# Optimization experiments

Hardware: AMD Instinct MI355X
Metric: run time of the kernel (lower is better)

## Reference

```python
import jax, jax.numpy as jnp
import numpy as np
from jax import lax

B = 16
A = 3
LEVEL_HW = [(200, 200), (100, 100), (50, 50), (25, 25)]
STRIDES = [4, 8, 16, 32]
SIZES = [32.0, 64.0, 128.0, 256.0]
RATIOS = np.array([0.5, 1.0, 2.0])
IMG_H = IMG_W = 800.0
PRE_NMS = 1000          # pre_nms_top_n (testing), applied per level
POST_NMS = 1000         # post_nms_top_n (testing)
NMS_THRESH = 0.7
SCORE_THRESH = 0.0
MIN_SIZE = 1.0
BBOX_XFORM_CLIP = float(np.log(1000.0 / 16.0))  # torchvision BoxCoder clamp
N_PER_LEVEL = [h * w * A for h, w in LEVEL_HW]


def _make_anchors():
    # torchvision-style grid anchors, per-location order matches (H, W, A) flatten
    out = []
    for (h, w), stride, size in zip(LEVEL_HW, STRIDES, SIZES):
        hr = np.sqrt(RATIOS)
        wr = 1.0 / hr
        ws = size * wr
        hs = size * hr
        base = np.stack([-ws / 2, -hs / 2, ws / 2, hs / 2], axis=1)  # [A,4]
        sx = np.arange(w) * stride
        sy = np.arange(h) * stride
        yy, xx = np.meshgrid(sy, sx, indexing="ij")
        shifts = np.stack([xx, yy, xx, yy], axis=-1).reshape(-1, 1, 4)
        out.append((shifts + base[None]).reshape(-1, 4))
    return np.concatenate(out, 0).astype(np.float32)


def setup_inputs():
    key = jax.random.key(0)
    ks = jax.random.split(key, 8)
    inp = {}
    for i, (h, w) in enumerate(LEVEL_HW):
        inp[f"cls{i}"] = jax.random.normal(ks[i], (B, A, h, w), jnp.float32)
        inp[f"reg{i}"] = jax.random.normal(ks[4 + i], (B, A * 4, h, w), jnp.float32)
    inp["anchors"] = jnp.asarray(_make_anchors())
    return inp


def _flat(layer, C):
    # permute_and_flatten: [N, A*C, H, W] -> [N, H*W*A, C]
    n, ac, h, w = layer.shape
    a = ac // C
    return layer.reshape(n, a, C, h, w).transpose(0, 3, 4, 1, 2).reshape(n, h * w * a, C)


def _forward(cls_list, reg_list, anchors):
    obj = jnp.concatenate([_flat(c, 1)[..., 0] for c in cls_list], axis=1)   # [B, K]
    deltas = jnp.concatenate([_flat(r, 4) for r in reg_list], axis=1)        # [B, K, 4]

    # --- BoxCoder.decode, weights (1,1,1,1) ---
    wa = anchors[:, 2] - anchors[:, 0]
    ha = anchors[:, 3] - anchors[:, 1]
    cxa = anchors[:, 0] + 0.5 * wa
    cya = anchors[:, 1] + 0.5 * ha
    dx, dy = deltas[..., 0], deltas[..., 1]
    dw = jnp.minimum(deltas[..., 2], BBOX_XFORM_CLIP)
    dh = jnp.minimum(deltas[..., 3], BBOX_XFORM_CLIP)
    pcx = dx * wa + cxa
    pcy = dy * ha + cya
    pw = jnp.exp(dw) * wa
    ph = jnp.exp(dh) * ha
    props = jnp.stack([pcx - 0.5 * pw, pcy - 0.5 * ph,
                       pcx + 0.5 * pw, pcy + 0.5 * ph], -1)  # [B, K, 4]

    # --- per-level top-k (pre_nms_top_n) ---
    idxs = []
    off = 0
    for n in N_PER_LEVEL:
        k = min(PRE_NMS, n)
        _, ti = lax.top_k(obj[:, off:off + n], k)
        idxs.append(ti + off)
        off += n
    top_idx = jnp.concatenate(idxs, axis=1)  # [B, Nc]
    lvl_full = jnp.concatenate([jnp.full((n,), i, jnp.int32)
                                for i, n in enumerate(N_PER_LEVEL)])
    scores = jax.nn.sigmoid(jnp.take_along_axis(obj, top_idx, axis=1))
    boxes = jnp.take_along_axis(props, top_idx[..., None], axis=1)
    lvl = lvl_full[top_idx]

    # --- clip to image, remove small boxes / score threshold (as validity mask) ---
    x1 = jnp.clip(boxes[..., 0], 0.0, IMG_W)
    y1 = jnp.clip(boxes[..., 1], 0.0, IMG_H)
    x2 = jnp.clip(boxes[..., 2], 0.0, IMG_W)
    y2 = jnp.clip(boxes[..., 3], 0.0, IMG_H)
    boxes = jnp.stack([x1, y1, x2, y2], -1)
    valid = (x2 - x1 >= MIN_SIZE) & (y2 - y1 >= MIN_SIZE) & (scores >= SCORE_THRESH)

    # --- sort by score desc (invalid ranked last) ---
    key = jnp.where(valid, scores, -1.0)
    order = jnp.argsort(-key, axis=1)
    boxes = jnp.take_along_axis(boxes, order[..., None], axis=1)
    scores = jnp.take_along_axis(scores, order, axis=1)
    lvl = jnp.take_along_axis(lvl, order, axis=1)
    valid = jnp.take_along_axis(valid, order, axis=1)

    # --- batched_nms: offset boxes by level so cross-level IoU = 0 ---
    off_mult = max(IMG_H, IMG_W) + 1.0
    boff = boxes + lvl[..., None].astype(boxes.dtype) * off_mult
    areas = (boff[..., 2] - boff[..., 0]) * (boff[..., 3] - boff[..., 1])  # [B, Nc]
    Nc = boff.shape[1]
    pos = jnp.arange(Nc)

    def step(supp, i):
        bi = boff[:, i]                                   # [B, 4]
        keep_i = valid[:, i] & (~supp[:, i])              # [B]
        ix1 = jnp.maximum(boff[..., 0], bi[:, None, 0])
        iy1 = jnp.maximum(boff[..., 1], bi[:, None, 1])
        ix2 = jnp.minimum(boff[..., 2], bi[:, None, 2])
        iy2 = jnp.minimum(boff[..., 3], bi[:, None, 3])
        inter = jnp.maximum(ix2 - ix1, 0.0) * jnp.maximum(iy2 - iy1, 0.0)
        union = areas + areas[:, i][:, None] - inter
        iou = inter / jnp.where(union > 0, union, 1.0)
        sup = keep_i[:, None] & (iou > NMS_THRESH) & (pos > i)[None, :]
        return supp | sup, keep_i

    _, keeps = lax.scan(step, jnp.zeros((boxes.shape[0], Nc), bool), pos)
    keep = keeps.T  # [B, Nc]

    # --- compact kept boxes (already score-sorted) into fixed [B, POST_NMS, ...] ---
    def sel(b, s, k):
        rank = jnp.cumsum(k) - 1
        idx = jnp.where(k & (rank < POST_NMS), rank, POST_NMS)  # overflow -> slot POST
        ob = jnp.zeros((POST_NMS + 1, 4), b.dtype).at[idx].set(b)[:POST_NMS]
        osc = jnp.zeros((POST_NMS + 1,), s.dtype).at[idx].set(s)[:POST_NMS]
        return ob, osc

    return jax.vmap(sel)(boxes, scores, keep)


def reference(cls0, cls1, cls2, cls3, reg0, reg1, reg2, reg3, anchors):
    return _forward([cls0, cls1, cls2, cls3], [reg0, reg1, reg2, reg3], anchors)
```

## Files before the change

### kernel.cpp

```cpp
#include <hip/hip_runtime.h>
#include <cstdint>
#include <cstddef>

typedef uint32_t u32;
typedef uint64_t u64;

#define NB 16
#define POSTN 1000
#define PREN 1000
#define LSEG 1024
#define LCH 16
#define SIDECAP 4096
#define BSIDE 2048
#define TRIPCAP (LSEG * LCH)
#define NPAIR 160
#define NBUCK 8192
#define BSHIFT 19

__constant__ int c_N[4]    = {120000, 30000, 7500, 1875};
__constant__ int c_OFF[4]  = {0, 120000, 150000, 157500};
__constant__ int c_HW[4]   = {40000, 10000, 2500, 625};
__constant__ int c_W[4]    = {200, 100, 50, 25};
__constant__ int c_BASE[4] = {0, 1024, 2048, 3072};

__device__ __forceinline__ u32 ord_bits(float f) {
  u32 u = __float_as_uint(f);
  return (u & 0x80000000u) ? ~u : (u | 0x80000000u);
}
__device__ __forceinline__ float inv_ord(u32 o) {
  u32 bits = (o & 0x80000000u) ? (o ^ 0x80000000u) : ~o;
  return __uint_as_float(bits);
}
__device__ __forceinline__ u64 readlane_u64(u64 v, int l) {
  u32 lo = (u32)__builtin_amdgcn_readlane((int)(u32)v, l);
  u32 hi = (u32)__builtin_amdgcn_readlane((int)(u32)(v >> 32), l);
  return (((u64)hi) << 32) | (u64)lo;
}

__device__ __forceinline__ void slice_map(int bid, int& lvl, int& b, int& e0,
                                          int& nsl) {
  if (bid < 128)      { lvl = 0; b = bid >> 3; e0 = (bid & 7) * 15000; nsl = 15000; }
  else if (bid < 160) { lvl = 1; int t = bid - 128; b = t >> 1; e0 = (t & 1) * 15000; nsl = 15000; }
  else if (bid < 176) { lvl = 2; b = bid - 160; e0 = 0; nsl = 7500; }
  else                { lvl = 3; b = bid - 176; e0 = 0; nsl = 1875; }
}

struct DecBox { float x1, y1, x2, y2; int lvl; bool valid; };

__device__ DecBox decode_box(u32 gid, int b,
    const float* __restrict__ reg0, const float* __restrict__ reg1,
    const float* __restrict__ reg2, const float* __restrict__ reg3,
    const float* __restrict__ anchors) {
  int lvl = (gid < 120000u) ? 0 : (gid < 150000u) ? 1 : (gid < 157500u) ? 2 : 3;
  int local = (int)gid - c_OFF[lvl];
  int a = local % 3;
  int cell = local / 3;
  int w = c_W[lvl];
  int hw = c_HW[lvl];
  int y = cell / w;
  int x = cell - y * w;
  const float* reg = (lvl == 0) ? reg0 : (lvl == 1) ? reg1 : (lvl == 2) ? reg2 : reg3;
  size_t base = ((size_t)(b * 12 + a * 4) * (size_t)w + (size_t)y) * (size_t)w + (size_t)x;
  const float CLIPV = 4.135166556742356f;
  float dx = reg[base];
  float dy = reg[base + (size_t)hw];
  float dwv = fminf(reg[base + 2 * (size_t)hw], CLIPV);
  float dhv = fminf(reg[base + 3 * (size_t)hw], CLIPV);
  float a0 = anchors[(size_t)gid * 4 + 0];
  float a1 = anchors[(size_t)gid * 4 + 1];
  float a2 = anchors[(size_t)gid * 4 + 2];
  float a3 = anchors[(size_t)gid * 4 + 3];
  float wa = __fsub_rn(a2, a0);
  float ha = __fsub_rn(a3, a1);
  float cxa = __fadd_rn(a0, __fmul_rn(0.5f, wa));
  float cya = __fadd_rn(a1, __fmul_rn(0.5f, ha));
  float pcx = __fadd_rn(__fmul_rn(dx, wa), cxa);
  float pcy = __fadd_rn(__fmul_rn(dy, ha), cya);
  float pw = __fmul_rn(expf(dwv), wa);
  float ph = __fmul_rn(expf(dhv), ha);
  float x1 = __fsub_rn(pcx, __fmul_rn(0.5f, pw));
  float y1 = __fsub_rn(pcy, __fmul_rn(0.5f, ph));
  float x2 = __fadd_rn(pcx, __fmul_rn(0.5f, pw));
  float y2 = __fadd_rn(pcy, __fmul_rn(0.5f, ph));
  x1 = fminf(fmaxf(x1, 0.0f), 800.0f);
  y1 = fminf(fmaxf(y1, 0.0f), 800.0f);
  x2 = fminf(fmaxf(x2, 0.0f), 800.0f);
  y2 = fminf(fmaxf(y2, 0.0f), 800.0f);
  DecBox r;
  r.x1 = x1; r.y1 = y1; r.x2 = x2; r.y2 = y2; r.lvl = lvl;
  r.valid = (__fsub_rn(x2, x1) >= 1.0f) && (__fsub_rn(y2, y1) >= 1.0f);
  return r;
}

__global__ void k_zero(float* __restrict__ out, u32* __restrict__ counters,
                       u32* __restrict__ sidecnt, u32* __restrict__ tripcnt,
                       u64* __restrict__ cand_key,
                       u32* __restrict__ hist1, u32* __restrict__ state_known,
                       u32* __restrict__ state_kneed) {
  int i = blockIdx.x * blockDim.x + threadIdx.x;
  if (i < NB * POSTN * 5) out[i] = 0.0f;
  if (i < NB * 4096) cand_key[i] = 0ull;
  if (i < 64 * NBUCK) hist1[i] = 0u;
  if (i < 64 * 16) { counters[i] = 0u; sidecnt[i] = 0u; tripcnt[i] = 0u; }
  if (i < 64) { state_known[i] = 0u; state_kneed[i] = (u32)PREN; }
}

__global__ __launch_bounds__(1024) void k_hist1(
    const float* __restrict__ cls0, const float* __restrict__ cls1,
    const float* __restrict__ cls2, const float* __restrict__ cls3,
    u32* __restrict__ hist1) {
  int lvl, b, e0, nsl;
  slice_map(blockIdx.x, lvl, b, e0, nsl);
  const float* cls = (lvl == 0) ? cls0 : (lvl == 1) ? cls1 : (lvl == 2) ? cls2 : cls3;
  const float* cp = cls + (size_t)b * c_N[lvl];
  int tid = threadIdx.x;
  __shared__ u32 h[NBUCK];
  for (int t = tid; t < NBUCK; t += 1024) h[t] = 0u;
  __syncthreads();
  if (lvl != 3) {
    const float4* cp4 = (const float4*)(cp + e0);
    int n4 = nsl >> 2;
    for (int t = tid; t < n4; t += 1024) {
      float4 v = cp4[t];
      atomicAdd(&h[ord_bits(v.x) >> BSHIFT], 1u);
      atomicAdd(&h[ord_bits(v.y) >> BSHIFT], 1u);
      atomicAdd(&h[ord_bits(v.z) >> BSHIFT], 1u);
      atomicAdd(&h[ord_bits(v.w) >> BSHIFT], 1u);
    }
  } else {
    for (int e = e0 + tid; e < e0 + nsl; e += 1024)
      atomicAdd(&h[ord_bits(cp[e]) >> BSHIFT], 1u);
  }
  __syncthreads();
  int task = lvl * 16 + b;
  for (int t = tid; t < NBUCK; t += 1024) {
    u32 v = h[t];
    if (v) atomicAdd(&hist1[task * NBUCK + t], v);
  }
}

__global__ __launch_bounds__(1024) void k_pick1(
    const u32* __restrict__ hist1, u32* __restrict__ state_known,
    u32* __restrict__ state_kneed) {
  int task = blockIdx.x;
  int tid = threadIdx.x;
  __shared__ u32 h[NBUCK];
  __shared__ u32 spA[1024];
  __shared__ u32 spB[1024];
  __shared__ int sh_t;
  __shared__ u32 sh_above;
  u32 kneed = (u32)PREN;
  for (int t = tid; t < NBUCK; t += 1024) h[t] = hist1[task * NBUCK + t];
  __syncthreads();
  int base = tid << 3;
  u32 part = 0;
#pragma unroll
  for (int j = 0; j < 8; ++j) part += h[base + j];
  spA[tid] = part;
  __syncthreads();
  u32* cur = spA;
  u32* nxt = spB;
  for (int off = 1; off < 1024; off <<= 1) {
    u32 v = cur[tid] + ((tid + off < 1024) ? cur[tid + off] : 0u);
    nxt[tid] = v;
    __syncthreads();
    u32* tmp = cur; cur = nxt; nxt = tmp;
  }
  u32 suf = (tid + 1 < 1024) ? cur[tid + 1] : 0u;
#pragma unroll
  for (int j = 7; j >= 0; --j) {
    u32 s = suf + h[base + j];
    if (s >= kneed && suf < kneed) { sh_t = base + j; sh_above = suf; }
    suf = s;
  }
  __syncthreads();
  if (tid == 0) {
    state_known[task] = (u32)sh_t << BSHIFT;
    state_kneed[task] = kneed - sh_above;
  }
}

__global__ __launch_bounds__(1024) void k_collect(
    const float* __restrict__ cls0, const float* __restrict__ cls1,
    const float* __restrict__ cls2, const float* __restrict__ cls3,
    const u32* __restrict__ state_known,
    const float* __restrict__ reg0, const float* __restrict__ reg1,
    const float* __restrict__ reg2, const float* __restrict__ reg3,
    const float* __restrict__ anchors, u32* __restrict__ counters,
    u32* __restrict__ sidecnt, u64* __restrict__ sidebuf,
    u64* __restrict__ cand_key) {
  int lvl, b, e0, nsl;
  slice_map(blockIdx.x, lvl, b, e0, nsl);
  int task = lvl * 16 + b;
  u32 tb = state_known[task] >> BSHIFT;
  const float* cls = (lvl == 0) ? cls0 : (lvl == 1) ? cls1 : (lvl == 2) ? cls2 : cls3;
  const float* cp = cls + (size_t)b * c_N[lvl];
  int tid = threadIdx.x;
  __shared__ u32 ldef[1024];
  __shared__ u32 lside[BSIDE];
  __shared__ u32 cdef, cside, bdef, bside;
  if (tid == 0) { cdef = 0u; cside = 0u; }
  __syncthreads();
  if (lvl != 3) {
    const float4* cp4 = (const float4*)(cp + e0);
    int n4 = nsl >> 2;
    for (int t = tid; t < n4; t += 1024) {
      float4 v4 = cp4[t];
      int ebase = e0 + (t << 2);
#pragma unroll
      for (int c = 0; c < 4; ++c) {
        float f = (c == 0) ? v4.x : (c == 1) ? v4.y : (c == 2) ? v4.z : v4.w;
        u32 bk = ord_bits(f) >> BSHIFT;
        if (bk < tb) continue;
        if (bk > tb) {
          u32 i = atomicAdd(&cdef, 1u);
          if (i < 1024u) ldef[i] = (u32)(ebase + c);
        } else {
          u32 i = atomicAdd(&cside, 1u);
          if (i < (u32)BSIDE) lside[i] = (u32)(ebase + c);
        }
      }
    }
  } else {
    for (int e = e0 + tid; e < e0 + nsl; e += 1024) {
      u32 bk = ord_bits(cp[e]) >> BSHIFT;
      if (bk < tb) continue;
      if (bk > tb) {
        u32 i = atomicAdd(&cdef, 1u);
        if (i < 1024u) ldef[i] = (u32)e;
      } else {
        u32 i = atomicAdd(&cside, 1u);
        if (i < (u32)BSIDE) lside[i] = (u32)e;
      }
    }
  }
  __syncthreads();
  if (tid == 0) bdef = atomicAdd(&counters[task * 16], min(cdef, 1024u));
  if (tid == 1) bside = atomicAdd(&sidecnt[task * 16], min(cside, (u32)BSIDE));
  __syncthreads();
  int hw = c_HW[lvl], off = c_OFF[lvl];
  u32 nd = min(cdef, 1024u);
  for (u32 i = tid; i < nd; i += 1024) {
    int e = (int)ldef[i];
    int a = e / hw;
    int cell = e - a * hw;
    u32 gid = (u32)(off + cell * 3 + a);
    u64 key = ((u64)ord_bits(cp[e]) << 32) | (u32)(~gid);
    DecBox bx = decode_box(gid, b, reg0, reg1, reg2, reg3, anchors);
    u64 skey = bx.valid ? key : (key & 0xFFFFFFFFull);
    u32 slot = bdef + i;
    if (slot < (u32)PREN)
      cand_key[(size_t)b * 4096 + c_BASE[lvl] + slot] = skey;
  }
  u32 ns = min(cside, (u32)BSIDE);
  for (u32 i = tid; i < ns; i += 1024) {
    int e = (int)lside[i];
    int a = e / hw;
    int cell = e - a * hw;
    u32 gid = (u32)(off + cell * 3 + a);
    u64 key = ((u64)ord_bits(cp[e]) << 32) | (u32)(~gid);
    u32 slot = bside + i;
    if (slot < (u32)SIDECAP) sidebuf[(size_t)task * SIDECAP + slot] = key;
  }
}

__global__ __launch_bounds__(1024) void k_sortdec(
    u64* __restrict__ cand_key, const u64* __restrict__ sidebuf,
    const u32* __restrict__ sidecnt, const u32* __restrict__ counters,
    const u32* __restrict__ state_kneed,
    const float* __restrict__ reg0, const float* __restrict__ reg1,
    const float* __restrict__ reg2, const float* __restrict__ reg3,
    const float* __restrict__ anchors,
    float4* __restrict__ sbox, float4* __restrict__ boffA,
    float* __restrict__ area, float* __restrict__ score,
    u64* __restrict__ vmaskl, u32* __restrict__ rnzl) {
  int bl = blockIdx.x;
  int b = bl >> 2;
  int lvl = bl & 3;
  int task = lvl * 16 + b;
  int tid = threadIdx.x;
  rnzl[(size_t)bl * LSEG + tid] = 0u;
  __shared__ u64 sside[SIDECAP];
  __shared__ u64 sk[LSEG];
  u32 nside = min(sidecnt[task * 16], (u32)SIDECAP);
  u32 kneed = state_kneed[task];
  u32 nab = counters[task * 16];
  u32 np2 = 64;
  while (np2 < nside) np2 <<= 1;
  for (u32 i = tid; i < np2; i += 1024)
    sside[i] = (i < nside) ? sidebuf[(size_t)task * SIDECAP + i] : 0ull;
  __syncthreads();
  for (u32 k = 2; k <= np2; k <<= 1) {
    for (u32 j = k >> 1; j > 0; j >>= 1) {
      for (u32 t = tid; t < np2 / 2; t += 1024) {
        u32 i = 2u * t - (t & (j - 1u));
        u32 l2 = i | j;
        u64 av = sside[i], bv = sside[l2];
        bool up = ((i & k) == 0u);
        if (up ? (av < bv) : (av > bv)) { sside[i] = bv; sside[l2] = av; }
      }
      __syncthreads();
    }
  }
  if (tid < (int)kneed) {
    u64 key = sside[tid];
    u32 gid = ~((u32)key);
    DecBox bx = decode_box(gid, b, reg0, reg1, reg2, reg3, anchors);
    sside[tid] = bx.valid ? key : (key & 0xFFFFFFFFull);
  }
  u64 defk = (tid < (int)nab)
                 ? cand_key[(size_t)b * 4096 + c_BASE[lvl] + tid] : 0ull;
  __syncthreads();
  u64 kv = defk;
  if (tid >= (int)nab && tid < (int)(nab + kneed)) kv = sside[tid - nab];
  sk[tid] = kv;
  __syncthreads();
  for (u32 k = 2; k <= LSEG; k <<= 1) {
    for (u32 j = k >> 1; j > 0; j >>= 1) {
      if (tid < LSEG / 2) {
        u32 t = (u32)tid;
        u32 i = 2u * t - (t & (j - 1u));
        u32 l2 = i | j;
        u64 av = sk[i], bv = sk[l2];
        bool up = ((i & k) == 0u);
        if (up ? (av < bv) : (av > bv)) { sk[i] = bv; sk[l2] = av; }
      }
      __syncthreads();
    }
  }
  u64 key = sk[tid];
  cand_key[(size_t)bl * LSEG + tid] = key;
  float4 bx4 = make_float4(0.f, 0.f, 0.f, 0.f);
  float4 bo4 = make_float4(0.f, 0.f, 0.f, 0.f);
  float ar = 0.f, sc = 0.f;
  bool vflag = false;
  if (key != 0ull) {
    u32 gid = ~((u32)key);
    vflag = (key >> 32) != 0ull;
    DecBox bx = decode_box(gid, b, reg0, reg1, reg2, reg3, anchors);
    bx4 = make_float4(bx.x1, bx.y1, bx.x2, bx.y2);
    float offv = __fmul_rn((float)bx.lvl, 801.0f);
    bo4 = make_float4(__fadd_rn(bx.x1, offv), __fadd_rn(bx.y1, offv),
                      __fadd_rn(bx.x2, offv), __fadd_rn(bx.y2, offv));
    ar = __fmul_rn(__fsub_rn(bo4.z, bo4.x), __fsub_rn(bo4.w, bo4.y));
    if (vflag) {
      float logit = inv_ord((u32)(key >> 32));
      sc = 1.0f / (1.0f + expf(-logit));
    }
  }
  size_t gi = (size_t)bl * LSEG + tid;
  sbox[gi] = bx4;
  boffA[gi] = bo4;
  area[gi] = ar;
  score[gi] = sc;
  u64 bal = __ballot(vflag ? 1 : 0);
  if ((tid & 63) == 0) vmaskl[bl * LCH + (tid >> 6)] = bal;
}

#define RPB 16
__global__ __launch_bounds__(256) void k_maskl(
    const float4* __restrict__ boffA, const float* __restrict__ area,
    ulonglong2* __restrict__ trip, u32* __restrict__ tripcnt,
    u32* __restrict__ rnzl) {
  const double Bd = 0x1.6666661p-1;
  int bg = blockIdx.x;
  int bl = bg / NPAIR;
  int p = bg - bl * NPAIR;
  int chunk, g;
  if (p < 16)      { chunk = 0; g = p; }
  else if (p < 48) { chunk = 1; g = p - 16; }
  else if (p < 96) { chunk = 2; g = p - 48; }
  else             { chunk = 3; g = p - 96; }
  int row0 = g * RPB;
  int tid = threadIdx.x;
  int wave = tid >> 6;
  int lane = tid & 63;
  __shared__ float4 rb[RPB];
  __shared__ float ra[RPB];
  __shared__ ulonglong2 stage[RPB * 4];
  __shared__ u32 scount, sbase;
  if (tid == 0) scount = 0u;
  if (tid < RPB) {
    rb[tid] = boffA[(size_t)bl * LSEG + row0 + tid];
    ra[tid] = area[(size_t)bl * LSEG + row0 + tid];
  }
  __syncthreads();
  int wword = chunk * 4 + wave;
  int wmaxj = chunk * 256 + wave * 64 + 63;
  int j = chunk * 256 + tid;
  float4 cb = boffA[(size_t)bl * LSEG + j];
  float ca = area[(size_t)bl * LSEG + j];
  if (wmaxj > row0) {
#pragma unroll
    for (int rr = 0; rr < RPB; ++rr) {
      int i = row0 + rr;
      if (wmaxj <= i) continue;
      float4 rbb = rb[rr];
      float ria = ra[rr];
      float ix1 = fmaxf(cb.x, rbb.x);
      float iy1 = fmaxf(cb.y, rbb.y);
      float ix2 = fminf(cb.z, rbb.z);
      float iy2 = fminf(cb.w, rbb.w);
      float inter = __fmul_rn(fmaxf(__fsub_rn(ix2, ix1), 0.0f),
                              fmaxf(__fsub_rn(iy2, iy1), 0.0f));
      float uni = __fsub_rn(__fadd_rn(ca, ria), inter);
      bool pred = (j > i) && (inter > 0.0f) &&
                  ((double)inter >= Bd * (double)uni);
      u64 bal = __ballot(pred ? 1 : 0);
      if (lane == 0 && bal) {
        u32 sidx = atomicAdd(&scount, 1u);
        ulonglong2 e;
        e.x = bal;
        e.y = (u64)(u32)(i * LCH + wword);
        stage[sidx] = e;
        atomicOr(&rnzl[(size_t)bl * LSEG + i], 1u << wword);
      }
    }
  }
  __syncthreads();
  if (tid == 0 && scount) sbase = atomicAdd(&tripcnt[bl * 16], scount);
  __syncthreads();
  for (u32 t = tid; t < scount; t += 256)
    trip[(size_t)bl * TRIPCAP + sbase + t] = stage[t];
}

__global__ __launch_bounds__(64) void k_nmsl(
    const ulonglong2* __restrict__ trip, const u32* __restrict__ tripcnt,
    const u32* __restrict__ rnzl, const u64* __restrict__ vmaskl,
    const u64* __restrict__ cand_key,
    u64* __restrict__ keptkeys, u32* __restrict__ keptpos,
    u32* __restrict__ keptcnt) {
  int bl = blockIdx.x;
  int lane = threadIdx.x;
  extern __shared__ char smem[];
  u64* lmask = (u64*)smem;
  u32* rnzL  = (u32*)(smem + (size_t)LSEG * LCH * 8);
  ulonglong2 z2; z2.x = 0ull; z2.y = 0ull;
  ulonglong2* lm2 = (ulonglong2*)lmask;
  for (int t = lane; t < LSEG * LCH / 2; t += 64) lm2[t] = z2;
  for (int t = lane; t < LSEG; t += 64) rnzL[t] = rnzl[(size_t)bl * LSEG + t];
  u64 vword = (lane < LCH) ? vmaskl[bl * LCH + lane] : 0ull;
  __syncthreads();
  u32 tc = tripcnt[bl * 16];
  for (u32 t = lane; t < tc; t += 64) {
    ulonglong2 e = trip[(size_t)bl * TRIPCAP + t];
    lmask[(u32)e.y] = e.x;
  }
  __syncthreads();
  u64 supp = 0ull;
  u64 keep = 0ull;
  for (int W = 0; W < LCH; ++W) {
    int c0 = W << 6;
    u32 rzW = rnzL[c0 + lane];
    u64 dchW = lmask[(size_t)(c0 + lane) * LCH + W];
    u64 s = __shfl(supp, W);
    u64 v = __shfl(vword, W);
    u64 pending = v & ~s;
    u64 kw = 0ull;
    u64 suppressors = __ballot((dchW & pending) != 0ull) & pending;
    while (pending) {
      u64 sp = pending & suppressors;
      if (!sp) { kw |= pending; break; }
      int q = __builtin_ctzll(sp);
      u64 below = pending & ((1ull << q) - 1ull);
      kw |= below | (1ull << q);
      u64 supq = readlane_u64(dchW, q);
      pending &= ~supq & ~below & ~(1ull << q);
    }
    u64 kk = __ballot(((rzW >> W) >> 1) != 0u) & kw;
    bool ld = (lane < LCH);
    u64 acc = 0ull;
    while (kk) {
      int q0 = __builtin_ctzll(kk); kk &= kk - 1ull;
      u64 m0 = ld ? lmask[(size_t)(c0 + q0) * LCH + lane] : 0ull;
      u64 m1 = 0ull, m2 = 0ull, m3 = 0ull;
      if (kk) {
        int q1 = __builtin_ctzll(kk); kk &= kk - 1ull;
        m1 = ld ? lmask[(size_t)(c0 + q1) * LCH + lane] : 0ull;
      }
      if (kk) {
        int q2 = __builtin_ctzll(kk); kk &= kk - 1ull;
        m2 = ld ? lmask[(size_t)(c0 + q2) * LCH + lane] : 0ull;
      }
      if (kk) {
        int q3 = __builtin_ctzll(kk); kk &= kk - 1ull;
        m3 = ld ? lmask[(size_t)(c0 + q3) * LCH + lane] : 0ull;
      }
      acc |= (m0 | m1) | (m2 | m3);
    }
    supp |= acc;
    if (lane == W) keep = kw;
  }
  int pc = __popcll(keep);
  int incl = pc;
  for (int d = 1; d < 64; d <<= 1) {
    int t = __shfl_up(incl, d);
    if (lane >= d) incl += t;
  }
  int r = incl - pc;
  u64 kk = keep;
  while (kk) {
    int bit = __builtin_ctzll(kk);
    kk &= kk - 1ull;
    int p = lane * 64 + bit;
    keptkeys[(size_t)bl * LSEG + r] = cand_key[(size_t)bl * LSEG + p];
    keptpos[(size_t)bl * LSEG + r] = (u32)p;
    ++r;
  }
  if (lane == 63) keptcnt[bl] = (u32)incl;
}

__global__ __launch_bounds__(1024) void k_out(
    const u64* __restrict__ keptkeys, const u32* __restrict__ keptpos,
    const u32* __restrict__ keptcnt, const float4* __restrict__ sbox,
    const float* __restrict__ score, float* __restrict__ out) {
  int bl = blockIdx.x;
  int b = bl >> 2;
  int l = bl & 3;
  int r = threadIdx.x;
  u32 cnt = keptcnt[bl];
  if (r >= (int)cnt) return;
  u64 K = keptkeys[(size_t)bl * LSEG + r];
  int rank = r;
#pragma unroll
  for (int dl = 0; dl < 4; ++dl) {
    if (dl == l) continue;
    int obl = (b << 2) | dl;
    const u64* arr = keptkeys + (size_t)obl * LSEG;
    int lo = 0, hi = (int)keptcnt[obl];
    while (lo < hi) {
      int mid = (lo + hi) >> 1;
      if (arr[mid] > K) lo = mid + 1; else hi = mid;
    }
    rank += lo;
  }
  if (rank < POSTN) {
    u32 p = keptpos[(size_t)bl * LSEG + r];
    float4 bx = sbox[(size_t)bl * LSEG + p];
    size_t ob = ((size_t)b * POSTN + (size_t)rank) * 4;
    out[ob + 0] = bx.x;
    out[ob + 1] = bx.y;
    out[ob + 2] = bx.z;
    out[ob + 3] = bx.w;
    out[(size_t)NB * POSTN * 4 + (size_t)b * POSTN + (size_t)rank] =
        score[(size_t)bl * LSEG + p];
  }
}

extern "C" void kernel_launch(void* const* d_in, const int* in_sizes, int n_in,
                              void* d_out, int out_size, void* d_ws, size_t ws_size,
                              hipStream_t stream) {
  const float* cls0 = (const float*)d_in[0];
  const float* reg0 = (const float*)d_in[1];
  const float* cls1 = (const float*)d_in[2];
  const float* reg1 = (const float*)d_in[3];
  const float* cls2 = (const float*)d_in[4];
  const float* reg2 = (const float*)d_in[5];
  const float* cls3 = (const float*)d_in[6];
  const float* reg3 = (const float*)d_in[7];
  const float* anchors = (const float*)d_in[8];
  float* out = (float*)d_out;

  char* ws = (char*)d_ws;
  size_t off = 0;
  auto take = [&](size_t bytes) -> void* {
    off = (off + 255) & ~(size_t)255;
    void* p = ws + off;
    off += bytes;
    return p;
  };
  ulonglong2* trip = (ulonglong2*)take((size_t)64 * TRIPCAP * 16);
  u64* sidebuf   = (u64*)take((size_t)64 * SIDECAP * 8);
  u32* rnzl      = (u32*)take((size_t)64 * LSEG * 4);
  u64* cand_key  = (u64*)take((size_t)NB * 4096 * 8);
  float4* sbox   = (float4*)take((size_t)64 * LSEG * 16);
  float4* boffA  = (float4*)take((size_t)64 * LSEG * 16);
  float* area    = (float*)take((size_t)64 * LSEG * 4);
  float* score   = (float*)take((size_t)64 * LSEG * 4);
  u64* vmaskl    = (u64*)take((size_t)64 * LCH * 8);
  u64* keptkeys  = (u64*)take((size_t)64 * LSEG * 8);
  u32* keptpos   = (u32*)take((size_t)64 * LSEG * 4);
  u32* keptcnt   = (u32*)take((size_t)64 * 4);
  u32* hist1     = (u32*)take((size_t)64 * NBUCK * 4);
  u32* counters  = (u32*)take((size_t)64 * 16 * 4);
  u32* sidecnt   = (u32*)take((size_t)64 * 16 * 4);
  u32* tripcnt   = (u32*)take((size_t)64 * 16 * 4);
  u32* state_known = (u32*)take((size_t)64 * 4);
  u32* state_kneed = (u32*)take((size_t)64 * 4);
  (void)ws_size; (void)in_sizes; (void)n_in; (void)out_size;

  k_zero<<<2048, 256, 0, stream>>>(out, counters, sidecnt, tripcnt, cand_key,
                                   hist1, state_known, state_kneed);
  k_hist1<<<192, 1024, 0, stream>>>(cls0, cls1, cls2, cls3, hist1);
  k_pick1<<<64, 1024, 0, stream>>>(hist1, state_known, state_kneed);
  k_collect<<<192, 1024, 0, stream>>>(cls0, cls1, cls2, cls3, state_known,
                                      reg0, reg1, reg2, reg3, anchors,
                                      counters, sidecnt, sidebuf, cand_key);
  k_sortdec<<<64, 1024, 0, stream>>>(cand_key, sidebuf, sidecnt, counters,
                                     state_kneed, reg0, reg1, reg2, reg3,
                                     anchors, sbox, boffA, area, score,
                                     vmaskl, rnzl);
  k_maskl<<<64 * NPAIR, 256, 0, stream>>>(boffA, area, trip, tripcnt, rnzl);
  k_nmsl<<<64, 64, 135168, stream>>>(trip, tripcnt, rnzl, vmaskl, cand_key,
                                     keptkeys, keptpos, keptcnt);
  k_out<<<64, 1024, 0, stream>>>(keptkeys, keptpos, keptcnt, sbox, score, out);
}
```

Baseline: 125.9 us.

## Fuse zeroing into histogram kernel and merge threshold pick into collect

Removes the separate zeroing kernel by folding buffer initialization into k_hist1, and removes k_pick1 by having each collect block reduce the per-slice histograms and compute the threshold bucket itself. Per-block histograms are written without global atomics, so hist1 no longer needs clearing. This cuts two kernel launches and the global atomic merge, at the cost of redundant suffix-scan work in every slice block of a task. The zeroing depends on enough threads in k_hist1 (192x1024 covers out and cand_key sizes).

```diff
diff --git a/kernel.cpp b/kernel.cpp
--- a/kernel.cpp
+++ b/kernel.cpp
@@ -43,6 +43,12 @@
   else if (bid < 160) { lvl = 1; int t = bid - 128; b = t >> 1; e0 = (t & 1) * 15000; nsl = 15000; }
   else if (bid < 176) { lvl = 2; b = bid - 160; e0 = 0; nsl = 7500; }
   else                { lvl = 3; b = bid - 176; e0 = 0; nsl = 1875; }
+}
+__device__ __forceinline__ void task_rows(int lvl, int b, int& row0, int& nrow) {
+  if (lvl == 0)      { row0 = b << 3;        nrow = 8; }
+  else if (lvl == 1) { row0 = 128 + (b << 1); nrow = 2; }
+  else if (lvl == 2) { row0 = 160 + b;        nrow = 1; }
+  else               { row0 = 176 + b;        nrow = 1; }
 }
 
 struct DecBox { float x1, y1, x2, y2; int lvl; bool valid; };
@@ -92,28 +98,24 @@
   return r;
 }
 
-__global__ void k_zero(float* __restrict__ out, u32* __restrict__ counters,
-                       u32* __restrict__ sidecnt, u32* __restrict__ tripcnt,
-                       u64* __restrict__ cand_key,
-                       u32* __restrict__ hist1, u32* __restrict__ state_known,
-                       u32* __restrict__ state_kneed) {
-  int i = blockIdx.x * blockDim.x + threadIdx.x;
-  if (i < NB * POSTN * 5) out[i] = 0.0f;
-  if (i < NB * 4096) cand_key[i] = 0ull;
-  if (i < 64 * NBUCK) hist1[i] = 0u;
-  if (i < 64 * 16) { counters[i] = 0u; sidecnt[i] = 0u; tripcnt[i] = 0u; }
-  if (i < 64) { state_known[i] = 0u; state_kneed[i] = (u32)PREN; }
-}
-
 __global__ __launch_bounds__(1024) void k_hist1(
     const float* __restrict__ cls0, const float* __restrict__ cls1,
     const float* __restrict__ cls2, const float* __restrict__ cls3,
-    u32* __restrict__ hist1) {
+    u32* __restrict__ histb, float* __restrict__ out,
+    u64* __restrict__ cand_key, u32* __restrict__ counters,
+    u32* __restrict__ sidecnt, u32* __restrict__ tripcnt,
+    u32* __restrict__ state_kneed) {
+  int bid = blockIdx.x;
+  int tid = threadIdx.x;
+  int g = bid * 1024 + tid;
+  if (g < NB * POSTN * 5) out[g] = 0.0f;
+  if (g < NB * 4096) cand_key[g] = 0ull;
+  if (g < 64 * 16) { counters[g] = 0u; sidecnt[g] = 0u; tripcnt[g] = 0u; }
+  if (g < 64) state_kneed[g] = (u32)PREN;
   int lvl, b, e0, nsl;
-  slice_map(blockIdx.x, lvl, b, e0, nsl);
+  slice_map(bid, lvl, b, e0, nsl);
   const float* cls = (lvl == 0) ? cls0 : (lvl == 1) ? cls1 : (lvl == 2) ? cls2 : cls3;
   const float* cp = cls + (size_t)b * c_N[lvl];
-  int tid = threadIdx.x;
   __shared__ u32 h[NBUCK];
   for (int t = tid; t < NBUCK; t += 1024) h[t] = 0u;
   __syncthreads();
@@ -132,26 +134,37 @@
       atomicAdd(&h[ord_bits(cp[e]) >> BSHIFT], 1u);
   }
   __syncthreads();
+  for (int t = tid; t < NBUCK; t += 1024)
+    histb[(size_t)bid * NBUCK + t] = h[t];
+}
+
+__global__ __launch_bounds__(1024) void k_collect(
+    const float* __restrict__ cls0, const float* __restrict__ cls1,
+    const float* __restrict__ cls2, const float* __restrict__ cls3,
+    const u32* __restrict__ histb,
+    const float* __restrict__ reg0, const float* __restrict__ reg1,
+    const float* __restrict__ reg2, const float* __restrict__ reg3,
+    const float* __restrict__ anchors, u32* __restrict__ counters,
+    u32* __restrict__ sidecnt, u64* __restrict__ sidebuf,
+    u64* __restrict__ cand_key, u32* __restrict__ state_kneed) {
+  int lvl, b, e0, nsl;
+  slice_map(blockIdx.x, lvl, b, e0, nsl);
   int task = lvl * 16 + b;
-  for (int t = tid; t < NBUCK; t += 1024) {
-    u32 v = h[t];
-    if (v) atomicAdd(&hist1[task * NBUCK + t], v);
-  }
-}
-
-__global__ __launch_bounds__(1024) void k_pick1(
-    const u32* __restrict__ hist1, u32* __restrict__ state_known,
-    u32* __restrict__ state_kneed) {
-  int task = blockIdx.x;
   int tid = threadIdx.x;
   __shared__ u32 h[NBUCK];
   __shared__ u32 spA[1024];
   __shared__ u32 spB[1024];
   __shared__ int sh_t;
   __shared__ u32 sh_above;
+  int row0r, nrow;
+  task_rows(lvl, b, row0r, nrow);
+  for (int t = tid; t < NBUCK; t += 1024) {
+    u32 s = 0;
+    for (int r = 0; r < nrow; ++r) s += histb[(size_t)(row0r + r) * NBUCK + t];
+    h[t] = s;
+  }
+  __syncthreads();
   u32 kneed = (u32)PREN;
-  for (int t = tid; t < NBUCK; t += 1024) h[t] = hist1[task * NBUCK + t];
-  __syncthreads();
   int base = tid << 3;
   u32 part = 0;
 #pragma unroll
@@ -174,28 +187,10 @@
     suf = s;
   }
   __syncthreads();
-  if (tid == 0) {
-    state_known[task] = (u32)sh_t << BSHIFT;
-    state_kneed[task] = kneed - sh_above;
-  }
-}
-
-__global__ __launch_bounds__(1024) void k_collect(
-    const float* __restrict__ cls0, const float* __restrict__ cls1,
-    const float* __restrict__ cls2, const float* __restrict__ cls3,
-    const u32* __restrict__ state_known,
-    const float* __restrict__ reg0, const float* __restrict__ reg1,
-    const float* __restrict__ reg2, const float* __restrict__ reg3,
-    const float* __restrict__ anchors, u32* __restrict__ counters,
-    u32* __restrict__ sidecnt, u64* __restrict__ sidebuf,
-    u64* __restrict__ cand_key) {
-  int lvl, b, e0, nsl;
-  slice_map(blockIdx.x, lvl, b, e0, nsl);
-  int task = lvl * 16 + b;
-  u32 tb = state_known[task] >> BSHIFT;
+  u32 tb = (u32)sh_t;
+  if (e0 == 0 && tid == 0) state_kneed[task] = kneed - sh_above;
   const float* cls = (lvl == 0) ? cls0 : (lvl == 1) ? cls1 : (lvl == 2) ? cls2 : cls3;
   const float* cp = cls + (size_t)b * c_N[lvl];
-  int tid = threadIdx.x;
   __shared__ u32 ldef[1024];
   __shared__ u32 lside[BSIDE];
   __shared__ u32 cdef, cside, bdef, bside;
@@ -581,21 +576,20 @@
   u64* keptkeys  = (u64*)take((size_t)64 * LSEG * 8);
   u32* keptpos   = (u32*)take((size_t)64 * LSEG * 4);
   u32* keptcnt   = (u32*)take((size_t)64 * 4);
-  u32* hist1     = (u32*)take((size_t)64 * NBUCK * 4);
+  u32* histb     = (u32*)take((size_t)192 * NBUCK * 4);
   u32* counters  = (u32*)take((size_t)64 * 16 * 4);
   u32* sidecnt   = (u32*)take((size_t)64 * 16 * 4);
   u32* tripcnt   = (u32*)take((size_t)64 * 16 * 4);
-  u32* state_known = (u32*)take((size_t)64 * 4);
   u32* state_kneed = (u32*)take((size_t)64 * 4);
   (void)ws_size; (void)in_sizes; (void)n_in; (void)out_size;
 
-  k_zero<<<2048, 256, 0, stream>>>(out, counters, sidecnt, tripcnt, cand_key,
-                                   hist1, state_known, state_kneed);
-  k_hist1<<<192, 1024, 0, stream>>>(cls0, cls1, cls2, cls3, hist1);
-  k_pick1<<<64, 1024, 0, stream>>>(hist1, state_known, state_kneed);
-  k_collect<<<192, 1024, 0, stream>>>(cls0, cls1, cls2, cls3, state_known,
+  k_hist1<<<192, 1024, 0, stream>>>(cls0, cls1, cls2, cls3, histb, out,
+                                    cand_key, counters, sidecnt, tripcnt,
+                                    state_kneed);
+  k_collect<<<192, 1024, 0, stream>>>(cls0, cls1, cls2, cls3, histb,
                                       reg0, reg1, reg2, reg3, anchors,
-                                      counters, sidecnt, sidebuf, cand_key);
+                                      counters, sidecnt, sidebuf, cand_key,
+                                      state_kneed);
   k_sortdec<<<64, 1024, 0, stream>>>(cand_key, sidebuf, sidecnt, counters,
                                      state_kneed, reg0, reg1, reg2, reg3,
                                      anchors, sbox, boffA, area, score,
```

After: 135.4 us. 7.5% more time.
